# Kernel tuning notes

Measured on AMD Instinct MI355X. Metric: run time of the kernel, lower is better.

Reference implementation:

```python
import jax, jax.numpy as jnp
import numpy as np

DELTA_PULL = 0.5
DELTA_PUSH = 1.5
EPS = 1e-6


def setup_inputs() -> dict:
    key = jax.random.key(0)
    k1, k2 = jax.random.split(key)
    B, C, H, W, K = 4, 16, 512, 512, 16
    embedding_maps = jax.random.normal(k1, (B, C, H, W), dtype=jnp.float32)
    instance_masks = jax.random.randint(k2, (B, K, H, W), 0, 2, dtype=jnp.int32)
    return {"embedding_maps": embedding_maps, "instance_masks": instance_masks}


def reference(embedding_maps, instance_masks):
    emb = embedding_maps                      # [B, C, H, W]
    m = (instance_masks > 0).astype(emb.dtype)  # [B, K, H, W]
    K = m.shape[1]

    # per-instance masked segment reductions over all H*W pixels
    counts = m.sum((-1, -2))                                   # [B, K]
    sums = jnp.einsum('bchw,bkhw->bkc', emb, m)                # [B, K, C]
    sq_sums = jnp.einsum('bchw,bkhw->bkc', emb * emb, m)       # [B, K, C]

    valid = counts > 0                                          # [B, K]
    safe_counts = jnp.maximum(counts, 1.0)
    means = sums / safe_counts[..., None]                       # [B, K, C] exact fg mean

    # sum over fg pixels of ||e - mean||^2 = sq_sum - 2*mean.sum + n*mean^2
    pull_k = (sq_sums - 2.0 * means * sums + counts[..., None] * means * means).sum(-1)
    pull_k = jnp.where(valid, pull_k / (counts + EPS), 0.0)     # [B, K]

    M = valid.sum(-1).astype(emb.dtype)                         # [B] num valid instances
    pull_b = pull_k.sum(-1) / jnp.maximum(M, 1.0)               # [B]

    # pairwise push between valid instance means (i < j)
    diff = means[:, :, None, :] - means[:, None, :, :]          # [B, K, K, C]
    dist = jnp.sqrt((diff * diff).sum(-1) + 1e-12)              # [B, K, K]
    iu = jnp.arange(K)
    pair = valid[:, :, None] & valid[:, None, :] & (iu[:, None] < iu[None, :])
    push_terms = jnp.where(pair, jnp.maximum(DELTA_PUSH - dist, 0.0) ** 2, 0.0)
    npairs = M * (M - 1.0) / 2.0
    push_b = jnp.where(M > 1.0, push_terms.sum((-1, -2)) / jnp.maximum(npairs, 1.0), 0.0)

    return (DELTA_PULL * pull_b + push_b).mean()
```

## Files before the change

kernel.cpp:

```cpp
#include <hip/hip_runtime.h>

#define BB 4
#define CC 16
#define KK 16
#define HWP (512 * 512)
#define TP 512
#define NTILES (HWP / TP)
#define THREADS 256
#define NSLICE 8
#define WSTOT (64 + 1024 + 1024)

typedef short bf16x8 __attribute__((ext_vector_type(8)));
typedef float f32x4 __attribute__((ext_vector_type(4)));

__device__ __forceinline__ float fmaxf_(float a, float b) { return a > b ? a : b; }

__device__ __forceinline__ unsigned short f2bf(float f) {
    unsigned u = __float_as_uint(f);
    u += 0x7FFFu + ((u >> 16) & 1u);
    return (unsigned short)(u >> 16);
}

__global__ __launch_bounds__(THREADS) void disc_mfma_kernel(
    const float* __restrict__ emb, const int* __restrict__ masks,
    float* __restrict__ ws)
{
    __shared__ __align__(16) unsigned short bits[TP];
    __shared__ int wcnt[4][KK];
    __shared__ float redbuf[4][64][8];

    const int tid = threadIdx.x;
    const int b = blockIdx.x / NTILES;
    const int tile = blockIdx.x % NTILES;
    const size_t tile0 = (size_t)tile * TP;
    float* slice = ws + (size_t)(blockIdx.x & (NSLICE - 1)) * WSTOT;

    const int2* mbase2 = (const int2*)(masks + (size_t)b * KK * HWP + tile0);
    unsigned v0 = 0, v1 = 0;
    #pragma unroll
    for (int k = 0; k < KK; ++k) {
        int2 mm = mbase2[(size_t)k * (HWP / 2) + tid];
        v0 |= (mm.x > 0 ? 1u : 0u) << k;
        v1 |= (mm.y > 0 ? 1u : 0u) << k;
    }
    ((unsigned*)bits)[tid] = v0 | (v1 << 16);

    const int lane = tid & 63;
    const int wave = tid >> 6;
    int mycnt = 0;
    #pragma unroll
    for (int k = 0; k < KK; ++k) {
        unsigned long long b0 = __ballot((v0 >> k) & 1u);
        unsigned long long b1 = __ballot((v1 >> k) & 1u);
        if (lane == k) mycnt = __popcll(b0) + __popcll(b1);
    }
    if (lane < KK) wcnt[wave][lane] = mycnt;
    __syncthreads();

    const int quad = lane >> 4;
    const int r = lane & 15;
    const float* ebase = emb + ((size_t)b * CC + r) * HWP + tile0;

    f32x4 acc_s = {0.f, 0.f, 0.f, 0.f};
    f32x4 acc_q = {0.f, 0.f, 0.f, 0.f};

    #pragma unroll
    for (int g = 0; g < 4; ++g) {
        const int p0 = wave * 128 + g * 32;

        uint4 bw = *(const uint4*)&bits[p0 + quad * 8];
        union { bf16x8 v; unsigned u[4]; } A;
        A.u[0] = ((bw.x >> r) & 0x00010001u) * 0x3F80u;
        A.u[1] = ((bw.y >> r) & 0x00010001u) * 0x3F80u;
        A.u[2] = ((bw.z >> r) & 0x00010001u) * 0x3F80u;
        A.u[3] = ((bw.w >> r) & 0x00010001u) * 0x3F80u;

        const float4* ep = (const float4*)(ebase + p0 + quad * 8);
        float4 f0 = ep[0], f1 = ep[1];
        const float e[8] = {f0.x, f0.y, f0.z, f0.w, f1.x, f1.y, f1.z, f1.w};
        union { bf16x8 v; unsigned short s[8]; } Bf, B2;
        #pragma unroll
        for (int i = 0; i < 8; ++i) {
            Bf.s[i] = f2bf(e[i]);
            B2.s[i] = f2bf(e[i] * e[i]);
        }

        acc_s = __builtin_amdgcn_mfma_f32_16x16x32_bf16(A.v, Bf.v, acc_s, 0, 0, 0);
        acc_q = __builtin_amdgcn_mfma_f32_16x16x32_bf16(A.v, B2.v, acc_q, 0, 0, 0);
    }

    #pragma unroll
    for (int j = 0; j < 4; ++j) {
        redbuf[wave][lane][j] = acc_s[j];
        redbuf[wave][lane][4 + j] = acc_q[j];
    }
    __syncthreads();

    for (int fi = tid; fi < 512; fi += THREADS) {
        const int l2 = fi >> 3, j = fi & 7;
        float v = redbuf[0][l2][j] + redbuf[1][l2][j] + redbuf[2][l2][j] + redbuf[3][l2][j];
        const int reg = j & 3, isq = j >> 2;
        const int krow = (l2 >> 4) * 4 + reg;
        const int ccol = l2 & 15;
        atomicAdd(&slice[64 + isq * 1024 + ((size_t)b * KK + krow) * CC + ccol], v);
    }
    if (tid < KK) {
        float ctot = (float)(wcnt[0][tid] + wcnt[1][tid] + wcnt[2][tid] + wcnt[3][tid]);
        atomicAdd(&slice[b * KK + tid], ctot);
    }
}

__global__ __launch_bounds__(256) void disc_finalize_kernel(
    const float* __restrict__ ws, float* __restrict__ out)
{
    __shared__ float red[WSTOT];
    __shared__ float means[BB][KK][CC];
    __shared__ float partial[BB];
    const int tid = threadIdx.x;

    for (int idx = tid; idx < WSTOT; idx += 256) {
        float t = 0.f;
        #pragma unroll
        for (int s = 0; s < NSLICE; ++s) t += ws[(size_t)s * WSTOT + idx];
        red[idx] = t;
    }
    __syncthreads();

    const float* red_cnt = red;
    const float* red_sum = red + 64;
    const float* red_sq  = red + 64 + 1024;

    const int b = tid >> 6;
    const int lane = tid & 63;

    const float DELTA_PULL = 0.5f;
    const float DELTA_PUSH = 1.5f;
    const float EPS = 1e-6f;

    float cntk = 0.f;
    bool valid = false;
    float pull_k = 0.f;
    if (lane < KK) {
        int k = lane;
        cntk = red_cnt[b * KK + k];
        valid = cntk > 0.f;
        float safe = fmaxf_(cntk, 1.f);
        float acc_sq = 0.f, acc_ss = 0.f;
        #pragma unroll
        for (int c = 0; c < CC; ++c) {
            float sv = red_sum[(b * KK + k) * CC + c];
            means[b][k][c] = sv / safe;
            acc_sq += red_sq[(b * KK + k) * CC + c];
            acc_ss += sv * sv;
        }
        if (valid) pull_k = (acc_sq - acc_ss / cntk) / (cntk + EPS);
    }

    unsigned long long bal = __ballot(lane < KK && valid);
    float M = (float)__popcll(bal);

    float ps = pull_k;
    #pragma unroll
    for (int d = 32; d >= 1; d >>= 1) ps += __shfl_xor(ps, d, 64);
    float pull_b = ps / fmaxf_(M, 1.f);

    __syncthreads();

    float push = 0.f;
    for (int t = lane; t < KK * KK; t += 64) {
        int i = t >> 4, j = t & 15;
        if (i < j && ((bal >> i) & 1ull) && ((bal >> j) & 1ull)) {
            float d2 = 1e-12f;
            #pragma unroll
            for (int c = 0; c < CC; ++c) {
                float df = means[b][i][c] - means[b][j][c];
                d2 = fmaf(df, df, d2);
            }
            float dist = sqrtf(d2);
            float h = fmaxf_(DELTA_PUSH - dist, 0.f);
            push += h * h;
        }
    }
    #pragma unroll
    for (int d = 32; d >= 1; d >>= 1) push += __shfl_xor(push, d, 64);

    if (lane == 0) {
        float npairs = M * (M - 1.f) * 0.5f;
        float push_b = (M > 1.f) ? push / fmaxf_(npairs, 1.f) : 0.f;
        partial[b] = DELTA_PULL * pull_b + push_b;
    }
    __syncthreads();
    if (tid == 0) {
        out[0] = (partial[0] + partial[1] + partial[2] + partial[3]) * 0.25f;
    }
}

extern "C" void kernel_launch(void* const* d_in, const int* in_sizes, int n_in,
                              void* d_out, int out_size, void* d_ws, size_t ws_size,
                              hipStream_t stream) {
    const float* emb = (const float*)d_in[0];
    const int* masks = (const int*)d_in[1];
    float* ws = (float*)d_ws;

    hipMemsetAsync(d_ws, 0, NSLICE * WSTOT * sizeof(float), stream);

    dim3 grid(BB * NTILES);
    disc_mfma_kernel<<<grid, THREADS, 0, stream>>>(emb, masks, ws);
    disc_finalize_kernel<<<1, 256, 0, stream>>>(ws, (float*)d_out);
}
```

Measured before the change: 158.0 us.

## Make waves independent: per-wave tiles, MFMA counts, direct atomics without block syncs

Each block now covers 1024 pixels, with each wave owning 256 pixels end to end. A wave packs its own masks into bits, computes instance counts with an extra MFMA against a ones vector instead of ballots, and atomically adds its accumulators straight into one of 16 workspace slices. This drops both __syncthreads and the shared-memory cross-wave reduction, and halves the block count. In exchange there are more global atomics per block, spread across more slices to limit contention. Counts are now accumulated in fp32 through MFMA, which stays exact at these magnitudes.

```diff
diff --git a/kernel.cpp b/kernel.cpp
--- a/kernel.cpp
+++ b/kernel.cpp
@@ -4,10 +4,11 @@
 #define CC 16
 #define KK 16
 #define HWP (512 * 512)
-#define TP 512
-#define NTILES (HWP / TP)
+#define TPB 1024
+#define TPW 256
+#define NTILES (HWP / TPB)
 #define THREADS 256
-#define NSLICE 8
+#define NSLICE 16
 #define WSTOT (64 + 1024 + 1024)
 
 typedef short bf16x8 __attribute__((ext_vector_type(8)));
@@ -25,48 +26,46 @@
     const float* __restrict__ emb, const int* __restrict__ masks,
     float* __restrict__ ws)
 {
-    __shared__ __align__(16) unsigned short bits[TP];
-    __shared__ int wcnt[4][KK];
-    __shared__ float redbuf[4][64][8];
+    __shared__ __align__(16) unsigned short bits[TPB];
 
     const int tid = threadIdx.x;
+    const int lane = tid & 63;
+    const int wave = tid >> 6;
     const int b = blockIdx.x / NTILES;
     const int tile = blockIdx.x % NTILES;
-    const size_t tile0 = (size_t)tile * TP;
-    float* slice = ws + (size_t)(blockIdx.x & (NSLICE - 1)) * WSTOT;
-
-    const int2* mbase2 = (const int2*)(masks + (size_t)b * KK * HWP + tile0);
-    unsigned v0 = 0, v1 = 0;
-    #pragma unroll
-    for (int k = 0; k < KK; ++k) {
-        int2 mm = mbase2[(size_t)k * (HWP / 2) + tid];
-        v0 |= (mm.x > 0 ? 1u : 0u) << k;
-        v1 |= (mm.y > 0 ? 1u : 0u) << k;
-    }
-    ((unsigned*)bits)[tid] = v0 | (v1 << 16);
-
-    const int lane = tid & 63;
-    const int wave = tid >> 6;
-    int mycnt = 0;
-    #pragma unroll
-    for (int k = 0; k < KK; ++k) {
-        unsigned long long b0 = __ballot((v0 >> k) & 1u);
-        unsigned long long b1 = __ballot((v1 >> k) & 1u);
-        if (lane == k) mycnt = __popcll(b0) + __popcll(b1);
-    }
-    if (lane < KK) wcnt[wave][lane] = mycnt;
-    __syncthreads();
+    const size_t tile0 = (size_t)tile * TPB;
+    const int wbase = wave * TPW;
+    float* slice = ws + (size_t)((blockIdx.x * 4 + wave) & (NSLICE - 1)) * WSTOT;
 
     const int quad = lane >> 4;
     const int r = lane & 15;
+
+    const int* mbase = masks + (size_t)b * KK * HWP + tile0 + wbase;
+    #pragma unroll
+    for (int c = 0; c < 2; ++c) {
+        unsigned v0 = 0, v1 = 0;
+        #pragma unroll
+        for (int k = 0; k < KK; ++k) {
+            int2 mm = *(const int2*)(mbase + (size_t)k * HWP + c * 128 + 2 * lane);
+            v0 |= (mm.x > 0 ? 1u : 0u) << k;
+            v1 |= (mm.y > 0 ? 1u : 0u) << k;
+        }
+        ((unsigned*)bits)[(wbase + c * 128) / 2 + lane] = v0 | (v1 << 16);
+    }
+
+    union { bf16x8 v; unsigned short s[8]; } Bones;
+    #pragma unroll
+    for (int i = 0; i < 8; ++i) Bones.s[i] = 0x3F80;
+
     const float* ebase = emb + ((size_t)b * CC + r) * HWP + tile0;
 
     f32x4 acc_s = {0.f, 0.f, 0.f, 0.f};
     f32x4 acc_q = {0.f, 0.f, 0.f, 0.f};
-
-    #pragma unroll
-    for (int g = 0; g < 4; ++g) {
-        const int p0 = wave * 128 + g * 32;
+    f32x4 acc_c = {0.f, 0.f, 0.f, 0.f};
+
+    #pragma unroll
+    for (int g = 0; g < TPW / 32; ++g) {
+        const int p0 = wbase + g * 32;
 
         uint4 bw = *(const uint4*)&bits[p0 + quad * 8];
         union { bf16x8 v; unsigned u[4]; } A;
@@ -87,26 +86,20 @@
 
         acc_s = __builtin_amdgcn_mfma_f32_16x16x32_bf16(A.v, Bf.v, acc_s, 0, 0, 0);
         acc_q = __builtin_amdgcn_mfma_f32_16x16x32_bf16(A.v, B2.v, acc_q, 0, 0, 0);
-    }
-
-    #pragma unroll
-    for (int j = 0; j < 4; ++j) {
-        redbuf[wave][lane][j] = acc_s[j];
-        redbuf[wave][lane][4 + j] = acc_q[j];
-    }
-    __syncthreads();
-
-    for (int fi = tid; fi < 512; fi += THREADS) {
-        const int l2 = fi >> 3, j = fi & 7;
-        float v = redbuf[0][l2][j] + redbuf[1][l2][j] + redbuf[2][l2][j] + redbuf[3][l2][j];
-        const int reg = j & 3, isq = j >> 2;
-        const int krow = (l2 >> 4) * 4 + reg;
-        const int ccol = l2 & 15;
-        atomicAdd(&slice[64 + isq * 1024 + ((size_t)b * KK + krow) * CC + ccol], v);
-    }
-    if (tid < KK) {
-        float ctot = (float)(wcnt[0][tid] + wcnt[1][tid] + wcnt[2][tid] + wcnt[3][tid]);
-        atomicAdd(&slice[b * KK + tid], ctot);
+        acc_c = __builtin_amdgcn_mfma_f32_16x16x32_bf16(A.v, Bones.v, acc_c, 0, 0, 0);
+    }
+
+    #pragma unroll
+    for (int reg = 0; reg < 4; ++reg) {
+        const int krow = quad * 4 + reg;
+        atomicAdd(&slice[64 + ((size_t)b * KK + krow) * CC + r], acc_s[reg]);
+        atomicAdd(&slice[64 + 1024 + ((size_t)b * KK + krow) * CC + r], acc_q[reg]);
+    }
+    if (r == 0) {
+        #pragma unroll
+        for (int reg = 0; reg < 4; ++reg) {
+            atomicAdd(&slice[b * KK + quad * 4 + reg], acc_c[reg]);
+        }
     }
 }
 
```

Result: no change. 157.2 us (-0.5%).
